# Optimization experiments

Hardware: AMD Instinct MI355X
Metric: run time of the kernel (lower is better)

Reference implementation:

```python
import jax, jax.numpy as jnp
import numpy as np

D_MODEL = 256; D_FFN = 2048; N_LEVELS = 4; N_HEADS = 8; N_POINTS = 4
B = 4; LQ = 900
SPATIAL_SHAPES = np.array([[100, 134], [50, 67], [25, 34], [13, 17]], dtype=np.int32)
LEVEL_START = np.concatenate([[0], np.cumsum(SPATIAL_SHAPES.prod(1))[:-1]]).astype(np.int32)
LV = int(SPATIAL_SHAPES.prod(1).sum())


def layer_norm(x, g, b, eps=1e-5):
    m = x.mean(-1, keepdims=True)
    v = ((x - m) ** 2).mean(-1, keepdims=True)
    return (x - m) / jnp.sqrt(v + eps) * g + b


def mha(x, in_w, in_b, out_w, out_b):
    # x: [L, B, C]  (seq-first, like nn.MultiheadAttention)
    L, Bm, C = x.shape
    dh = C // N_HEADS
    qkv = x @ in_w.T + in_b
    q, k, v = jnp.split(qkv, 3, axis=-1)
    q = q.reshape(L, Bm, N_HEADS, dh) / jnp.sqrt(jnp.asarray(dh, x.dtype))
    k = k.reshape(L, Bm, N_HEADS, dh)
    v = v.reshape(L, Bm, N_HEADS, dh)
    attn = jax.nn.softmax(jnp.einsum('lbhd,mbhd->bhlm', q, k), axis=-1)
    o = jnp.einsum('bhlm,mbhd->lbhd', attn, v).reshape(L, Bm, C)
    return o @ out_w.T + out_b


def bilinear_sample(value_l, x, y, Hl, Wl):
    # value_l: [BH, Hl*Wl, Dh]; x, y: [BH, S] in pixel coords (align_corners=False, zero pad)
    x0 = jnp.floor(x)
    y0 = jnp.floor(y)
    out = 0.0
    for dx, dy in ((0, 0), (1, 0), (0, 1), (1, 1)):
        xi = x0 + dx
        yi = y0 + dy
        wgt = (1.0 - jnp.abs(x - xi)) * (1.0 - jnp.abs(y - yi))
        valid = (xi >= 0) & (xi < Wl) & (yi >= 0) & (yi < Hl)
        xi_c = jnp.clip(xi, 0, Wl - 1).astype(jnp.int32)
        yi_c = jnp.clip(yi, 0, Hl - 1).astype(jnp.int32)
        idx = yi_c * Wl + xi_c  # [BH, S]
        v = jnp.take_along_axis(value_l, idx[..., None], axis=1)  # [BH, S, Dh]
        out = out + jnp.where(valid, wgt, 0.0)[..., None] * v
    return out


def msdeform(query, ref, mem, spatial_shapes, vproj_w, vproj_b, off_w, off_b, aw_w, aw_b, oproj_w, oproj_b):
    # query: [B, Lq, C]; ref: [B, Lq, L, 2] in [0,1]; mem: [B, Lv, C]
    Bm, Lq, C = query.shape
    Dh = C // N_HEADS
    value = (mem @ vproj_w.T + vproj_b).reshape(Bm, -1, N_HEADS, Dh)
    off = (query @ off_w.T + off_b).reshape(Bm, Lq, N_HEADS, N_LEVELS, N_POINTS, 2)
    aw = jax.nn.softmax((query @ aw_w.T + aw_b).reshape(Bm, Lq, N_HEADS, N_LEVELS * N_POINTS), axis=-1)
    aw = aw.reshape(Bm, Lq, N_HEADS, N_LEVELS, N_POINTS)
    norm = jnp.stack([spatial_shapes[:, 1], spatial_shapes[:, 0]], -1).astype(query.dtype)  # [L,2]=(W,H)
    loc = ref[:, :, None, :, None, :] + off / norm[None, None, None, :, None, :]  # [B,Lq,H,L,P,2]
    acc = jnp.zeros((Bm, Lq, N_HEADS, Dh), query.dtype)
    for l in range(N_LEVELS):
        Hl = int(SPATIAL_SHAPES[l, 0]); Wl = int(SPATIAL_SHAPES[l, 1]); s = int(LEVEL_START[l])
        v_l = value[:, s:s + Hl * Wl].transpose(0, 2, 1, 3).reshape(Bm * N_HEADS, Hl * Wl, Dh)
        x = (loc[:, :, :, l, :, 0] * Wl - 0.5).transpose(0, 2, 1, 3).reshape(Bm * N_HEADS, Lq * N_POINTS)
        y = (loc[:, :, :, l, :, 1] * Hl - 0.5).transpose(0, 2, 1, 3).reshape(Bm * N_HEADS, Lq * N_POINTS)
        sampled = bilinear_sample(v_l, x, y, Hl, Wl).reshape(Bm, N_HEADS, Lq, N_POINTS, Dh)
        acc = acc + jnp.einsum('bqhp,bhqpd->bqhd', aw[:, :, :, l], sampled)
    return acc.reshape(Bm, Lq, C) @ oproj_w.T + oproj_b


def forward_layer(tgt, tgt_reference_points, memory, memory_spatial_shapes,
                  vproj_w, vproj_b, off_w, off_b, aw_w, aw_b, oproj_w, oproj_b, ln1_g, ln1_b,
                  sa_in_w, sa_in_b, sa_out_w, sa_out_b, ln2_g, ln2_b,
                  l1_w, l1_b, l2_w, l2_b, ln3_g, ln3_b,
                  sa3_in_w, sa3_in_b, sa3_out_w, sa3_out_b, ln5_g, ln5_b,
                  l31_w, l31_b, l32_w, l32_b, ln33_g, ln33_b):
    # module_seq hardcoded in __init__: ['ca', 'sa', 'ffn', 'sa3', 'ffn3']; dropout = eval-mode identity
    # ---- ca (MSDeformAttn cross-attention) ----
    q = tgt.transpose(1, 0, 2)                                   # [B,LQ,C]
    ref = tgt_reference_points.transpose(1, 0, 2, 3)             # [B,LQ,L,2]
    mem = memory.transpose(1, 0, 2)                              # [B,LV,C]
    tgt2 = msdeform(q, ref, mem, memory_spatial_shapes, vproj_w, vproj_b, off_w, off_b,
                    aw_w, aw_b, oproj_w, oproj_b).transpose(1, 0, 2)
    tgt = layer_norm(tgt + tgt2, ln1_g, ln1_b)
    # ---- sa ----
    tgt = layer_norm(tgt + mha(tgt, sa_in_w, sa_in_b, sa_out_w, sa_out_b), ln2_g, ln2_b)
    # ---- ffn ----
    tgt = layer_norm(tgt + (jax.nn.relu(tgt @ l1_w.T + l1_b) @ l2_w.T + l2_b), ln3_g, ln3_b)
    # ---- sa3 ----
    tgt = layer_norm(tgt + mha(tgt, sa3_in_w, sa3_in_b, sa3_out_w, sa3_out_b), ln5_g, ln5_b)
    # ---- ffn3 ----
    tgt = layer_norm(tgt + (jax.nn.relu(tgt @ l31_w.T + l31_b) @ l32_w.T + l32_b), ln33_g, ln33_b)
    return tgt


def setup_inputs() -> dict:
    key = jax.random.key(0)
    ks = iter(jax.random.split(key, 48))
    def w(shape, s=0.02):
        return jax.random.normal(next(ks), shape, jnp.float32) * s
    C = D_MODEL; HLP = N_HEADS * N_LEVELS * N_POINTS
    z = lambda n: jnp.zeros((n,), jnp.float32)
    o = lambda n: jnp.ones((n,), jnp.float32)
    return {
        'tgt': w((LQ, B, C), 1.0),
        'tgt_reference_points': jax.random.uniform(next(ks), (LQ, B, N_LEVELS, 2), jnp.float32),
        'memory': w((LV, B, C), 1.0),
        'memory_spatial_shapes': jnp.asarray(SPATIAL_SHAPES),
        'memory_level_start_index': jnp.asarray(LEVEL_START),
        'vproj_w': w((C, C)), 'vproj_b': z(C),
        'off_w': w((HLP * 2, C)), 'off_b': w((HLP * 2,), 0.5),
        'aw_w': w((HLP, C)), 'aw_b': z(HLP),
        'oproj_w': w((C, C)), 'oproj_b': z(C),
        'ln1_g': o(C), 'ln1_b': z(C),
        'sa_in_w': w((3 * C, C)), 'sa_in_b': z(3 * C),
        'sa_out_w': w((C, C)), 'sa_out_b': z(C),
        'ln2_g': o(C), 'ln2_b': z(C),
        'l1_w': w((D_FFN, C)), 'l1_b': z(D_FFN),
        'l2_w': w((C, D_FFN)), 'l2_b': z(C),
        'ln3_g': o(C), 'ln3_b': z(C),
        'sa3_in_w': w((3 * C, C)), 'sa3_in_b': z(3 * C),
        'sa3_out_w': w((C, C)), 'sa3_out_b': z(C),
        'ln5_g': o(C), 'ln5_b': z(C),
        'l31_w': w((D_FFN, C)), 'l31_b': z(D_FFN),
        'l32_w': w((C, D_FFN)), 'l32_b': z(C),
        'ln33_g': o(C), 'ln33_b': z(C),
    }


def reference(tgt, tgt_reference_points, memory, memory_spatial_shapes, memory_level_start_index,
              vproj_w, vproj_b, off_w, off_b, aw_w, aw_b, oproj_w, oproj_b, ln1_g, ln1_b,
              sa_in_w, sa_in_b, sa_out_w, sa_out_b, ln2_g, ln2_b,
              l1_w, l1_b, l2_w, l2_b, ln3_g, ln3_b,
              sa3_in_w, sa3_in_b, sa3_out_w, sa3_out_b, ln5_g, ln5_b,
              l31_w, l31_b, l32_w, l32_b, ln33_g, ln33_b):
    return forward_layer(tgt, tgt_reference_points, memory, memory_spatial_shapes,
                         vproj_w, vproj_b, off_w, off_b, aw_w, aw_b, oproj_w, oproj_b, ln1_g, ln1_b,
                         sa_in_w, sa_in_b, sa_out_w, sa_out_b, ln2_g, ln2_b,
                         l1_w, l1_b, l2_w, l2_b, ln3_g, ln3_b,
                         sa3_in_w, sa3_in_b, sa3_out_w, sa3_out_b, ln5_g, ln5_b,
                         l31_w, l31_b, l32_w, l32_b, ln33_g, ln33_b)
```

## Files before the change

kernel.cpp:

```cpp
#include <hip/hip_runtime.h>
#include <math.h>

#define C 256
#define DH 32
#define NH 8
#define NL 4
#define NP 4
#define BQ 4
#define LQ 900
#define LVTOT 17821
#define DFFN 2048
#define NTOK (BQ*LQ)

typedef __attribute__((ext_vector_type(8))) short bf8_t;
typedef __attribute__((ext_vector_type(4))) float f4_t;
typedef __attribute__((ext_vector_type(8))) unsigned short us8_t;
typedef __attribute__((ext_vector_type(4))) unsigned short us4_t;

union U8 { us8_t v; unsigned int u[4]; };
union U4 { us4_t v; unsigned int u[2]; };

__device__ __forceinline__ unsigned short f2bf(float f) {
    unsigned int u = __float_as_uint(f);
    u += 0x7fffu + ((u >> 16) & 1u);
    return (unsigned short)(u >> 16);
}
__device__ __forceinline__ float b2f(unsigned short u) {
    return __uint_as_float(((unsigned int)u) << 16);
}
__device__ __forceinline__ unsigned int cvtpk(float lo, float hi) {
    unsigned int r;
    asm("v_cvt_pk_bf16_f32 %0, %1, %2" : "=v"(r) : "v"(lo), "v"(hi));
    return r;
}

#define WOFF_OFFAW   0
#define WOFF_VPROJ   98304
#define WOFF_OPROJ   163840
#define WOFF_SAIN    229376
#define WOFF_SAOUT   425984
#define WOFF_L1      491520
#define WOFF_L2      1015808
#define WOFF_SA3IN   1540096
#define WOFF_SA3OUT  1736704
#define WOFF_L31     1802240
#define WOFF_L32     2326528
#define WTOT         2850816
#define PTOT         (WTOT + 921600)

__global__ void k_prep(const float* __restrict__ off_w, const float* __restrict__ aw_w,
                       const float* __restrict__ vproj_w, const float* __restrict__ oproj_w,
                       const float* __restrict__ sa_in_w, const float* __restrict__ sa_out_w,
                       const float* __restrict__ l1_w, const float* __restrict__ l2_w,
                       const float* __restrict__ sa3_in_w, const float* __restrict__ sa3_out_w,
                       const float* __restrict__ l31_w, const float* __restrict__ l32_w,
                       const float* __restrict__ off_b, const float* __restrict__ aw_b,
                       const float* __restrict__ tgt,
                       unsigned short* __restrict__ Wbf, float* __restrict__ bias384,
                       unsigned short* __restrict__ tgtU) {
    int i = blockIdx.x * 256 + threadIdx.x;
    if (i < 384) bias384[i] = (i < 256) ? off_b[i] : aw_b[i - 256];
    if (i >= PTOT) return;
    if (i >= WTOT) { int j = i - WTOT; tgtU[j] = f2bf(tgt[j]); return; }
    const float* src; int rel;
    if      (i < WOFF_VPROJ)  { if (i < 65536) { src = off_w; rel = i; } else { src = aw_w; rel = i - 65536; } }
    else if (i < WOFF_OPROJ)  { src = vproj_w;  rel = i - WOFF_VPROJ; }
    else if (i < WOFF_SAIN)   { src = oproj_w;  rel = i - WOFF_OPROJ; }
    else if (i < WOFF_SAOUT)  { src = sa_in_w;  rel = i - WOFF_SAIN; }
    else if (i < WOFF_L1)     { src = sa_out_w; rel = i - WOFF_SAOUT; }
    else if (i < WOFF_L2)     { src = l1_w;     rel = i - WOFF_L1; }
    else if (i < WOFF_SA3IN)  { src = l2_w;     rel = i - WOFF_L2; }
    else if (i < WOFF_SA3OUT) { src = sa3_in_w; rel = i - WOFF_SA3IN; }
    else if (i < WOFF_L31)    { src = sa3_out_w; rel = i - WOFF_SA3OUT; }
    else if (i < WOFF_L32)    { src = l31_w;    rel = i - WOFF_L31; }
    else                      { src = l32_w;    rel = i - WOFF_L32; }
    Wbf[i] = f2bf(src[rel]);
}

enum { MODE_NORMAL = 0, MODE_RELU = 1, MODE_VALUE = 2, MODE_QKV = 3 };

#define LDP 40

template<int K, int KS, int NTOT, int MODE, int AB, int OB, int XCDG, int SPLITK>
__global__ void k_mgemm(const void* __restrict__ A_, const unsigned short* __restrict__ Wbf,
                        const float* __restrict__ bias, void* __restrict__ Y_,
                        void* __restrict__ Y2_, int nrows) {
    __shared__ unsigned short Ash[2][128 * LDP];
    __shared__ unsigned short Bsh[2][64 * LDP];
    int t = threadIdx.x;
    int lane = t & 63, w = t >> 6;
    int wm = w & 1, wn = w >> 1;
    int rbx, cbx, khoff = 0;
    if (SPLITK) {
        int blk = blockIdx.x;
        rbx = (blk >> 6) * 8 + (blk & 7);
        cbx = (blk >> 3) & 3;
        int half = (blk >> 5) & 1;
        khoff = half * K;
        if (half) { Y_ = Y2_; bias = nullptr; }
        if (rbx * 128 >= nrows) return;
    } else if (XCDG) {
        int blk = blockIdx.x;
        rbx = (blk >> 5) * 8 + (blk & 7);
        cbx = (blk >> 3) & 3;
        if (rbx * 128 >= nrows) return;
    } else {
        rbx = blockIdx.x;
        cbx = blockIdx.y;
    }
    int r0 = rbx * 128;
    int c0 = cbx * 64;

    f4_t acc[4][2];
#pragma unroll
    for (int mt = 0; mt < 4; ++mt)
#pragma unroll
        for (int nt = 0; nt < 2; ++nt) acc[mt][nt] = (f4_t)0.f;

    int arow = t >> 1;
    int akoff = (t & 1) * 16;
    int asrc = min(r0 + arow, nrows - 1);
    const float* aptrf = (const float*)A_ + (size_t)asrc * KS + akoff + khoff;
    const unsigned short* aptrh = (const unsigned short*)A_ + (size_t)asrc * KS + akoff + khoff;
    unsigned short* adst0 = &Ash[0][arow * LDP + akoff];
    unsigned short* adst1 = &Ash[1][arow * LDP + akoff];

    int brow = t >> 2;
    int bkoff = (t & 3) * 8;
    const unsigned short* bptr = Wbf + (size_t)(c0 + brow) * KS + bkoff + khoff;
    unsigned short* bdst0 = &Bsh[0][brow * LDP + bkoff];
    unsigned short* bdst1 = &Bsh[1][brow * LDP + bkoff];

    int lr = lane & 15, kg = lane >> 4;

    float4 fA0, fA1, fA2, fA3, gA0, gA1, gA2, gA3;
    us8_t hA0, hA1, hB0, hB1;
    us8_t wA, wB;

#define ISSUE_A(k0) do { \
        if (AB) { hA0 = *(const us8_t*)(aptrh + (k0)); hA1 = *(const us8_t*)(aptrh + (k0) + 8); } \
        else { fA0 = *(const float4*)(aptrf + (k0)); fA1 = *(const float4*)(aptrf + (k0) + 4); \
               fA2 = *(const float4*)(aptrf + (k0) + 8); fA3 = *(const float4*)(aptrf + (k0) + 12); } \
        wA = *(const us8_t*)(bptr + (k0)); } while (0)
#define ISSUE_B(k0) do { \
        if (AB) { hB0 = *(const us8_t*)(aptrh + (k0)); hB1 = *(const us8_t*)(aptrh + (k0) + 8); } \
        else { gA0 = *(const float4*)(aptrf + (k0)); gA1 = *(const float4*)(aptrf + (k0) + 4); \
               gA2 = *(const float4*)(aptrf + (k0) + 8); gA3 = *(const float4*)(aptrf + (k0) + 12); } \
        wB = *(const us8_t*)(bptr + (k0)); } while (0)
#define STORE_A(buf) do { \
        if (AB) { *(us8_t*)(adst##buf) = hA0; *(us8_t*)(adst##buf + 8) = hA1; } \
        else { U8 x, y; \
               x.u[0] = cvtpk(fA0.x, fA0.y); x.u[1] = cvtpk(fA0.z, fA0.w); \
               x.u[2] = cvtpk(fA1.x, fA1.y); x.u[3] = cvtpk(fA1.z, fA1.w); \
               y.u[0] = cvtpk(fA2.x, fA2.y); y.u[1] = cvtpk(fA2.z, fA2.w); \
               y.u[2] = cvtpk(fA3.x, fA3.y); y.u[3] = cvtpk(fA3.z, fA3.w); \
               *(us8_t*)(adst##buf) = x.v; *(us8_t*)(adst##buf + 8) = y.v; } \
        *(us8_t*)(bdst##buf) = wA; } while (0)
#define STORE_B(buf) do { \
        if (AB) { *(us8_t*)(adst##buf) = hB0; *(us8_t*)(adst##buf + 8) = hB1; } \
        else { U8 x, y; \
               x.u[0] = cvtpk(gA0.x, gA0.y); x.u[1] = cvtpk(gA0.z, gA0.w); \
               x.u[2] = cvtpk(gA1.x, gA1.y); x.u[3] = cvtpk(gA1.z, gA1.w); \
               y.u[0] = cvtpk(gA2.x, gA2.y); y.u[1] = cvtpk(gA2.z, gA2.w); \
               y.u[2] = cvtpk(gA3.x, gA3.y); y.u[3] = cvtpk(gA3.z, gA3.w); \
               *(us8_t*)(adst##buf) = x.v; *(us8_t*)(adst##buf + 8) = y.v; } \
        *(us8_t*)(bdst##buf) = wB; } while (0)
#define COMPUTE(buf) do { \
        bf8_t afr[4], bfr[2]; \
        _Pragma("unroll") \
        for (int mt = 0; mt < 4; ++mt) \
            afr[mt] = *(const bf8_t*)&Ash[buf][(wm * 64 + mt * 16 + lr) * LDP + kg * 8]; \
        _Pragma("unroll") \
        for (int nt = 0; nt < 2; ++nt) \
            bfr[nt] = *(const bf8_t*)&Bsh[buf][(wn * 32 + nt * 16 + lr) * LDP + kg * 8]; \
        _Pragma("unroll") \
        for (int mt = 0; mt < 4; ++mt) \
            _Pragma("unroll") \
            for (int nt = 0; nt < 2; ++nt) \
                acc[mt][nt] = __builtin_amdgcn_mfma_f32_16x16x32_bf16(afr[mt], bfr[nt], acc[mt][nt], 0, 0, 0); \
    } while (0)

    ISSUE_A(0);
#pragma unroll 1
    for (int k0 = 0; k0 < K; k0 += 64) {
        STORE_A(0);
        ISSUE_B(k0 + 32);
        __syncthreads();
        COMPUTE(0);
        STORE_B(1);
        if (k0 + 64 < K) ISSUE_A(k0 + 64);
        __syncthreads();
        COMPUTE(1);
    }
#undef ISSUE_A
#undef ISSUE_B
#undef STORE_A
#undef STORE_B
#undef COMPUTE

#pragma unroll
    for (int mt = 0; mt < 4; ++mt) {
#pragma unroll
        for (int nt = 0; nt < 2; ++nt) {
            int col = c0 + wn * 32 + nt * 16 + lr;
            float b0s = bias ? bias[col] : 0.f;
#pragma unroll
            for (int rr = 0; rr < 4; ++rr) {
                int row = r0 + wm * 64 + mt * 16 + kg * 4 + rr;
                if (row >= nrows) continue;
                float v = acc[mt][nt][rr] + b0s;
                size_t idx;
                if (MODE == MODE_NORMAL) {
                    idx = (size_t)row * NTOT + col;
                } else if (MODE == MODE_RELU) {
                    v = fmaxf(v, 0.f);
                    idx = (size_t)row * NTOT + col;
                } else if (MODE == MODE_VALUE) {
                    int lv = row >> 2, b = row & 3;
                    int h = col >> 5, d = col & 31;
                    idx = (((size_t)b * NH + h) * LVTOT + lv) * DH + d;
                } else {
                    int lq = row >> 2, b = row & 3;
                    int part = col >> 8, cc = col & 255;
                    int h = cc >> 5, d = cc & 31;
                    if (part == 0) v *= 0.17677669529663687f;
                    idx = (size_t)part * (BQ * NH * LQ * DH) + (((size_t)b * NH + h) * LQ + lq) * DH + d;
                }
                if (OB) ((unsigned short*)Y_)[idx] = f2bf(v);
                else    ((float*)Y_)[idx] = v;
            }
        }
    }
}

__global__ void k_sample(const float* __restrict__ trp, const float* __restrict__ offaw,
                         const unsigned short* __restrict__ value,
                         unsigned short* __restrict__ accU) {
    int r = blockIdx.x;
    int b = r & 3;
    int t = threadIdx.x;
    int h = t >> 5;
    int lane32 = t & 31;
    int l = lane32 >> 3;
    int dl = lane32 & 7;
    int d0 = dl * 4;
    const unsigned short* vb = value + ((size_t)b * NH + h) * (size_t)LVTOT * DH;

    const float* lg = offaw + (size_t)r * 384 + 256 + h * 16;
    float e0,e1,e2,e3,e4,e5,e6,e7,e8,e9,e10,e11,e12,e13,e14,e15;
    {
        float4 q0 = *(const float4*)(lg);
        float4 q1 = *(const float4*)(lg + 4);
        float4 q2 = *(const float4*)(lg + 8);
        float4 q3 = *(const float4*)(lg + 12);
        float mx = fmaxf(fmaxf(fmaxf(q0.x,q0.y),fmaxf(q0.z,q0.w)),
                   fmaxf(fmaxf(fmaxf(q1.x,q1.y),fmaxf(q1.z,q1.w)),
                   fmaxf(fmaxf(fmaxf(q2.x,q2.y),fmaxf(q2.z,q2.w)),
                         fmaxf(fmaxf(q3.x,q3.y),fmaxf(q3.z,q3.w)))));
        e0=__expf(q0.x-mx); e1=__expf(q0.y-mx); e2=__expf(q0.z-mx); e3=__expf(q0.w-mx);
        e4=__expf(q1.x-mx); e5=__expf(q1.y-mx); e6=__expf(q1.z-mx); e7=__expf(q1.w-mx);
        e8=__expf(q2.x-mx); e9=__expf(q2.y-mx); e10=__expf(q2.z-mx); e11=__expf(q2.w-mx);
        e12=__expf(q3.x-mx); e13=__expf(q3.y-mx); e14=__expf(q3.z-mx); e15=__expf(q3.w-mx);
    }
    float ssum = ((e0+e1)+(e2+e3)) + ((e4+e5)+(e6+e7)) + ((e8+e9)+(e10+e11)) + ((e12+e13)+(e14+e15));
    float sinv = 1.0f / ssum;
    float w0 = (l==0) ? e0 : (l==1) ? e4 : (l==2) ? e8  : e12;
    float w1 = (l==0) ? e1 : (l==1) ? e5 : (l==2) ? e9  : e13;
    float w2 = (l==0) ? e2 : (l==1) ? e6 : (l==2) ? e10 : e14;
    float w3 = (l==0) ? e3 : (l==1) ? e7 : (l==2) ? e11 : e15;
    w0 *= sinv; w1 *= sinv; w2 *= sinv; w3 *= sinv;

    int Hl = (l==0) ? 100 : (l==1) ? 50 : (l==2) ? 25 : 13;
    int Wl = (l==0) ? 134 : (l==1) ? 67 : (l==2) ? 34 : 17;
    int s  = (l==0) ? 0 : (l==1) ? 13400 : (l==2) ? 16750 : 17600;
    float fW = (float)Wl, fH = (float)Hl;

    float rx = trp[((size_t)r * NL + l) * 2 + 0];
    float ry = trp[((size_t)r * NL + l) * 2 + 1];
    const float* offr = offaw + (size_t)r * 384 + h * 32 + l * 8;

    float o0 = 0.f, o1 = 0.f, o2 = 0.f, o3 = 0.f;
#pragma unroll
    for (int p = 0; p < 4; ++p) {
        float ox = offr[p * 2 + 0];
        float oy = offr[p * 2 + 1];
        float wq = (p==0) ? w0 : (p==1) ? w1 : (p==2) ? w2 : w3;
        float x = (rx + ox / fW) * fW - 0.5f;
        float y = (ry + oy / fH) * fH - 0.5f;
        float x0 = floorf(x), y0 = floorf(y);
#pragma unroll
        for (int dy = 0; dy < 2; ++dy) {
#pragma unroll
            for (int dx = 0; dx < 2; ++dx) {
                float xi = x0 + dx, yi = y0 + dy;
                float wgt = (1.0f - fabsf(x - xi)) * (1.0f - fabsf(y - yi));
                bool valid = (xi >= 0.f) && (xi < fW) && (yi >= 0.f) && (yi < fH);
                int xic = min(max((int)xi, 0), Wl - 1);
                int yic = min(max((int)yi, 0), Hl - 1);
                float cw = (valid ? wgt : 0.f) * wq;
                us4_t v4 = *(const us4_t*)&vb[((size_t)(s + yic * Wl + xic)) * DH + d0];
                o0 += cw * b2f(v4[0]);
                o1 += cw * b2f(v4[1]);
                o2 += cw * b2f(v4[2]);
                o3 += cw * b2f(v4[3]);
            }
        }
    }
    o0 += __shfl_xor(o0, 8, 32); o0 += __shfl_xor(o0, 16, 32);
    o1 += __shfl_xor(o1, 8, 32); o1 += __shfl_xor(o1, 16, 32);
    o2 += __shfl_xor(o2, 8, 32); o2 += __shfl_xor(o2, 16, 32);
    o3 += __shfl_xor(o3, 8, 32); o3 += __shfl_xor(o3, 16, 32);
    if (l == 0) {
        U4 u;
        u.u[0] = cvtpk(o0, o1);
        u.u[1] = cvtpk(o2, o3);
        *(us4_t*)&accU[(size_t)r * C + h * 32 + d0] = u.v;
    }
}

__global__ void k_res_ln(const float* __restrict__ Y0, const float* __restrict__ Y1,
                         const float* __restrict__ Xres, const float* __restrict__ g,
                         const float* __restrict__ be, float* __restrict__ out,
                         unsigned short* __restrict__ outU) {
    int t = threadIdx.x, wv = t >> 6, lane = t & 63;
    int r = blockIdx.x * 4 + wv;
    float4 v = ((const float4*)(Y0 + (size_t)r * C))[lane];
    float4 x = ((const float4*)(Xres + (size_t)r * C))[lane];
    v.x += x.x; v.y += x.y; v.z += x.z; v.w += x.w;
    if (Y1) {
        float4 y1 = ((const float4*)(Y1 + (size_t)r * C))[lane];
        v.x += y1.x; v.y += y1.y; v.z += y1.z; v.w += y1.w;
    }
    float s = (v.x + v.y) + (v.z + v.w);
#pragma unroll
    for (int o = 32; o > 0; o >>= 1) s += __shfl_xor(s, o, 64);
    float mean = s * (1.0f / C);
    float4 dv = make_float4(v.x - mean, v.y - mean, v.z - mean, v.w - mean);
    float q = (dv.x * dv.x + dv.y * dv.y) + (dv.z * dv.z + dv.w * dv.w);
#pragma unroll
    for (int o = 32; o > 0; o >>= 1) q += __shfl_xor(q, o, 64);
    float rstd = rsqrtf(q * (1.0f / C) + 1e-5f);
    float4 g4 = ((const float4*)g)[lane];
    float4 b4 = ((const float4*)be)[lane];
    float4 o4 = make_float4(dv.x * rstd * g4.x + b4.x, dv.y * rstd * g4.y + b4.y,
                            dv.z * rstd * g4.z + b4.z, dv.w * rstd * g4.w + b4.w);
    ((float4*)(out + (size_t)r * C))[lane] = o4;
    if (outU) {
        U4 u;
        u.u[0] = cvtpk(o4.x, o4.y);
        u.u[1] = cvtpk(o4.z, o4.w);
        *(us4_t*)(outU + (size_t)r * C + lane * 4) = u.v;
    }
}

#define NQC3 15

__global__ __launch_bounds__(256, 1)
void k_attn3(const unsigned short* __restrict__ Q, const unsigned short* __restrict__ K,
             const unsigned short* __restrict__ V, unsigned short* __restrict__ O) {
    __shared__ unsigned short sK[4][64 * 72];
    __shared__ unsigned short sV[4][32 * 72];
    __shared__ float sPO[4][64 * 36];
    __shared__ float sWm[4][64], sWl[4][64];

    int blk = blockIdx.x;
    int bh = blk & 31;
    int qc = blk >> 5;
    int b = bh >> 3, h = bh & 7;
    int t = threadIdx.x;
    int w = t >> 6, lane = t & 63;
    int lr = lane & 15, g = lane >> 4;

    const unsigned short* Qb = Q + (size_t)bh * LQ * DH;
    const unsigned short* Kb = K + (size_t)bh * LQ * DH;
    const unsigned short* Vb = V + (size_t)bh * LQ * DH;

    unsigned short* Ks = sK[w];
    unsigned short* Vt = sV[w];
    unsigned short* Ps = (unsigned short*)sPO[w];

    bf8_t qf[4];
#pragma unroll
    for (int nt = 0; nt < 4; ++nt) {
        int qg = min(qc * 64 + nt * 16 + lr, LQ - 1);
        qf[nt] = *(const bf8_t*)(Qb + (size_t)qg * DH + g * 8);
    }

    float m[4], l[4];
    f4_t acc[2][4];
#pragma unroll
    for (int nt = 0; nt < 4; ++nt) {
        m[nt] = -3e38f; l[nt] = 0.f;
        acc[0][nt] = (f4_t)0.f; acc[1][nt] = (f4_t)0.f;
    }

    for (int ci = 0; ci < 4; ++ci) {
        int k0 = ci * 256 + w * 64;
        if (k0 >= LQ) break;
        int kgl = min(k0 + lane, LQ - 1);
        const unsigned short* kr = Kb + (size_t)kgl * DH;
        const unsigned short* vr = Vb + (size_t)kgl * DH;
#pragma unroll
        for (int i = 0; i < 4; ++i)
            *(us8_t*)&Ks[lane * 72 + i * 8] = *(const us8_t*)(kr + i * 8);
#pragma unroll
        for (int i = 0; i < 4; ++i) {
            us8_t v8 = *(const us8_t*)(vr + i * 8);
#pragma unroll
            for (int j = 0; j < 8; ++j)
                Vt[(i * 8 + j) * 72 + lane] = v8[j];
        }
        bf8_t ka[4];
#pragma unroll
        for (int mt = 0; mt < 4; ++mt)
            ka[mt] = *(const bf8_t*)&Ks[(mt * 16 + lr) * 72 + g * 8];
        f4_t st[4][4];
#pragma unroll
        for (int mt = 0; mt < 4; ++mt)
#pragma unroll
            for (int nt = 0; nt < 4; ++nt)
                st[mt][nt] = __builtin_amdgcn_mfma_f32_16x16x32_bf16(ka[mt], qf[nt], (f4_t)0.f, 0, 0, 0);
#pragma unroll
        for (int nt = 0; nt < 4; ++nt) {
            float sv[4][4];
            float cm = -3e38f;
#pragma unroll
            for (int mt = 0; mt < 4; ++mt)
#pragma unroll
                for (int rr = 0; rr < 4; ++rr) {
                    bool valid = (k0 + mt * 16 + g * 4 + rr) < LQ;
                    float s = valid ? st[mt][nt][rr] : -3e38f;
                    sv[mt][rr] = s;
                    cm = fmaxf(cm, s);
                }
            cm = fmaxf(cm, __shfl_xor(cm, 16, 64));
            cm = fmaxf(cm, __shfl_xor(cm, 32, 64));
            float mn = fmaxf(m[nt], cm);
            float sc = __expf(m[nt] - mn);
            float cs = 0.f;
#pragma unroll
            for (int mt = 0; mt < 4; ++mt) {
                float pv0 = (sv[mt][0] > -1e37f) ? __expf(sv[mt][0] - mn) : 0.f;
                float pv1 = (sv[mt][1] > -1e37f) ? __expf(sv[mt][1] - mn) : 0.f;
                float pv2 = (sv[mt][2] > -1e37f) ? __expf(sv[mt][2] - mn) : 0.f;
                float pv3 = (sv[mt][3] > -1e37f) ? __expf(sv[mt][3] - mn) : 0.f;
                cs += (pv0 + pv1) + (pv2 + pv3);
                U4 pk;
                pk.u[0] = cvtpk(pv0, pv1);
                pk.u[1] = cvtpk(pv2, pv3);
                *(us4_t*)&Ps[(nt * 16 + lr) * 72 + mt * 16 + g * 4] = pk.v;
            }
            cs += __shfl_xor(cs, 16, 64);
            cs += __shfl_xor(cs, 32, 64);
            l[nt] = l[nt] * sc + cs;
            m[nt] = mn;
            acc[0][nt] *= sc;
            acc[1][nt] *= sc;
        }
        bf8_t va[2][2];
#pragma unroll
        for (int md = 0; md < 2; ++md)
#pragma unroll
            for (int kt = 0; kt < 2; ++kt)
                va[md][kt] = *(const bf8_t*)&Vt[(md * 16 + lr) * 72 + kt * 32 + g * 8];
#pragma unroll
        for (int nt = 0; nt < 4; ++nt)
#pragma unroll
            for (int kt = 0; kt < 2; ++kt) {
                bf8_t pb = *(const bf8_t*)&Ps[(nt * 16 + lr) * 72 + kt * 32 + g * 8];
                acc[0][nt] = __builtin_amdgcn_mfma_f32_16x16x32_bf16(va[0][kt], pb, acc[0][nt], 0, 0, 0);
                acc[1][nt] = __builtin_amdgcn_mfma_f32_16x16x32_bf16(va[1][kt], pb, acc[1][nt], 0, 0, 0);
            }
    }

    if (g == 0) {
#pragma unroll
        for (int nt = 0; nt < 4; ++nt) {
            sWm[w][nt * 16 + lr] = m[nt];
            sWl[w][nt * 16 + lr] = l[nt];
        }
    }
    __syncthreads();
    float* ob = sPO[w];
#pragma unroll
    for (int nt = 0; nt < 4; ++nt) {
        int q = nt * 16 + lr;
        float M = fmaxf(fmaxf(sWm[0][q], sWm[1][q]), fmaxf(sWm[2][q], sWm[3][q]));
        float fac = __expf(m[nt] - M);
        f4_t v0 = acc[0][nt] * fac;
        f4_t v1 = acc[1][nt] * fac;
        *(f4_t*)&ob[q * 36 + g * 4] = v0;
        *(f4_t*)&ob[q * 36 + 16 + g * 4] = v1;
    }
    __syncthreads();
    {
        int q = t >> 2, d0 = (t & 3) * 8;
        int qglob = qc * 64 + q;
        if (qglob < LQ) {
            float M = fmaxf(fmaxf(sWm[0][q], sWm[1][q]), fmaxf(sWm[2][q], sWm[3][q]));
            float L = 0.f;
#pragma unroll
            for (int w2 = 0; w2 < 4; ++w2) L += sWl[w2][q] * __expf(sWm[w2][q] - M);
            float inv = 1.0f / L;
            f4_t r0 = (f4_t)0.f, r1 = (f4_t)0.f;
#pragma unroll
            for (int w2 = 0; w2 < 4; ++w2) {
                r0 += *(f4_t*)&sPO[w2][q * 36 + d0];
                r1 += *(f4_t*)&sPO[w2][q * 36 + d0 + 4];
            }
            r0 *= inv; r1 *= inv;
            U8 u;
            u.u[0] = cvtpk(r0[0], r0[1]);
            u.u[1] = cvtpk(r0[2], r0[3]);
            u.u[2] = cvtpk(r1[0], r1[1]);
            u.u[3] = cvtpk(r1[2], r1[3]);
            *(us8_t*)(O + ((size_t)(qglob * BQ + b)) * C + h * 32 + d0) = u.v;
        }
    }
}

extern "C" void kernel_launch(void* const* d_in, const int* in_sizes, int n_in,
                              void* d_out, int out_size, void* d_ws, size_t ws_size,
                              hipStream_t stream) {
    const float* tgt      = (const float*)d_in[0];
    const float* trp      = (const float*)d_in[1];
    const float* memory   = (const float*)d_in[2];
    const float* vproj_w  = (const float*)d_in[5];  const float* vproj_b  = (const float*)d_in[6];
    const float* off_w    = (const float*)d_in[7];  const float* off_b    = (const float*)d_in[8];
    const float* aw_w     = (const float*)d_in[9];  const float* aw_b     = (const float*)d_in[10];
    const float* oproj_w  = (const float*)d_in[11]; const float* oproj_b  = (const float*)d_in[12];
    const float* ln1_g    = (const float*)d_in[13]; const float* ln1_b    = (const float*)d_in[14];
    const float* sa_in_w  = (const float*)d_in[15]; const float* sa_in_b  = (const float*)d_in[16];
    const float* sa_out_w = (const float*)d_in[17]; const float* sa_out_b = (const float*)d_in[18];
    const float* ln2_g    = (const float*)d_in[19]; const float* ln2_b    = (const float*)d_in[20];
    const float* l1_w     = (const float*)d_in[21]; const float* l1_b     = (const float*)d_in[22];
    const float* l2_w     = (const float*)d_in[23]; const float* l2_b     = (const float*)d_in[24];
    const float* ln3_g    = (const float*)d_in[25]; const float* ln3_b    = (const float*)d_in[26];
    const float* sa3_in_w = (const float*)d_in[27]; const float* sa3_in_b = (const float*)d_in[28];
    const float* sa3_out_w= (const float*)d_in[29]; const float* sa3_out_b= (const float*)d_in[30];
    const float* ln5_g    = (const float*)d_in[31]; const float* ln5_b    = (const float*)d_in[32];
    const float* l31_w    = (const float*)d_in[33]; const float* l31_b    = (const float*)d_in[34];
    const float* l32_w    = (const float*)d_in[35]; const float* l32_b    = (const float*)d_in[36];
    const float* ln33_g   = (const float*)d_in[37]; const float* ln33_b   = (const float*)d_in[38];

    float* ws = (float*)d_ws;
    float* X              = ws;
    unsigned short* valueU= (unsigned short*)(ws + 921600);
    float* offaw          = ws + 10045952;
    unsigned short* accU  = (unsigned short*)(ws + 11428352);
    unsigned short* QKVu  = (unsigned short*)(ws + 12349952);
    unsigned short* Ou    = (unsigned short*)(ws + 13732352);
    unsigned short* H1u   = (unsigned short*)(ws + 14193152);
    float* Y              = ws + 17879552;
    float* Y2             = ws + 18801152;
    float* T1             = ws + 19722752;
    unsigned short* Wbf   = (unsigned short*)(ws + 20644352);
    float* bias384        = ws + 22069760;
    unsigned short* XU    = (unsigned short*)(ws + 22070144);
    unsigned short* tgtU  = (unsigned short*)(ws + 22530944);

    const int NVROWS = BQ * LVTOT;
    dim3 blk(256);
    dim3 gTok(29, 4);
    void* nullv = nullptr;

    k_prep<<<(PTOT + 255) / 256, blk, 0, stream>>>(off_w, aw_w, vproj_w, oproj_w, sa_in_w, sa_out_w,
                                                   l1_w, l2_w, sa3_in_w, sa3_out_w, l31_w, l32_w,
                                                   off_b, aw_b, tgt, Wbf, bias384, tgtU);

    k_mgemm<256, 256, 256, MODE_VALUE, 0, 1, 4, 0><<<70 * 32, blk, 0, stream>>>(memory, Wbf + WOFF_VPROJ, vproj_b, valueU, nullv, NVROWS);
    k_mgemm<256, 256, 384, MODE_NORMAL, 1, 0, 0, 0><<<dim3(29, 6), blk, 0, stream>>>(tgtU, Wbf + WOFF_OFFAW, bias384, offaw, nullv, NTOK);
    k_sample<<<NTOK, blk, 0, stream>>>(trp, offaw, valueU, accU);
    k_mgemm<256, 256, 256, MODE_NORMAL, 1, 0, 0, 0><<<gTok, blk, 0, stream>>>(accU, Wbf + WOFF_OPROJ, oproj_b, T1, nullv, NTOK);
    k_res_ln<<<NTOK / 4, blk, 0, stream>>>(T1, nullptr, tgt, ln1_g, ln1_b, X, XU);

    k_mgemm<256, 256, 768, MODE_QKV, 1, 1, 0, 0><<<dim3(29, 12), blk, 0, stream>>>(XU, Wbf + WOFF_SAIN, sa_in_b, QKVu, nullv, NTOK);
    k_attn3<<<32 * NQC3, blk, 0, stream>>>(QKVu, QKVu + 921600, QKVu + 1843200, Ou);
    k_mgemm<256, 256, 256, MODE_NORMAL, 1, 0, 0, 0><<<gTok, blk, 0, stream>>>(Ou, Wbf + WOFF_SAOUT, sa_out_b, T1, nullv, NTOK);
    k_res_ln<<<NTOK / 4, blk, 0, stream>>>(T1, nullptr, X, ln2_g, ln2_b, X, XU);

    k_mgemm<256, 256, 2048, MODE_RELU, 1, 1, 0, 0><<<dim3(29, 32), blk, 0, stream>>>(XU, Wbf + WOFF_L1, l1_b, H1u, nullv, NTOK);
    k_mgemm<1024, 2048, 256, MODE_NORMAL, 1, 0, 0, 1><<<4 * 64, blk, 0, stream>>>(H1u, Wbf + WOFF_L2, l2_b, Y, Y2, NTOK);
    k_res_ln<<<NTOK / 4, blk, 0, stream>>>(Y, Y2, X, ln3_g, ln3_b, X, XU);

    k_mgemm<256, 256, 768, MODE_QKV, 1, 1, 0, 0><<<dim3(29, 12), blk, 0, stream>>>(XU, Wbf + WOFF_SA3IN, sa3_in_b, QKVu, nullv, NTOK);
    k_attn3<<<32 * NQC3, blk, 0, stream>>>(QKVu, QKVu + 921600, QKVu + 1843200, Ou);
    k_mgemm<256, 256, 256, MODE_NORMAL, 1, 0, 0, 0><<<gTok, blk, 0, stream>>>(Ou, Wbf + WOFF_SA3OUT, sa3_out_b, T1, nullv, NTOK);
    k_res_ln<<<NTOK / 4, blk, 0, stream>>>(T1, nullptr, X, ln5_g, ln5_b, X, XU);

    k_mgemm<256, 256, 2048, MODE_RELU, 1, 1, 0, 0><<<dim3(29, 32), blk, 0, stream>>>(XU, Wbf + WOFF_L31, l31_b, H1u, nullv, NTOK);
    k_mgemm<1024, 2048, 256, MODE_NORMAL, 1, 0, 0, 1><<<4 * 64, blk, 0, stream>>>(H1u, Wbf + WOFF_L32, l32_b, Y, Y2, NTOK);
    k_res_ln<<<NTOK / 4, blk, 0, stream>>>(Y, Y2, X, ln33_g, ln33_b, (float*)d_out, nullptr);
}
```

Measured before the change: 264.8 us.

## Deepen GEMM global-load prefetch to four register stages

Restructures the GEMM main loop from a 2-stage register prefetch into a 4-stage one. Global loads for the next four K-slices are in flight while the current slice is computed from double-buffered LDS. The loop now steps K by 128 and needs K to be a multiple of 128. This hides more global memory latency at the cost of many more live registers, which could lower occupancy.

```diff
diff --git a/kernel.cpp b/kernel.cpp
--- a/kernel.cpp
+++ b/kernel.cpp
@@ -133,38 +133,25 @@
 
     int lr = lane & 15, kg = lane >> 4;
 
-    float4 fA0, fA1, fA2, fA3, gA0, gA1, gA2, gA3;
-    us8_t hA0, hA1, hB0, hB1;
-    us8_t wA, wB;
-
-#define ISSUE_A(k0) do { \
-        if (AB) { hA0 = *(const us8_t*)(aptrh + (k0)); hA1 = *(const us8_t*)(aptrh + (k0) + 8); } \
-        else { fA0 = *(const float4*)(aptrf + (k0)); fA1 = *(const float4*)(aptrf + (k0) + 4); \
-               fA2 = *(const float4*)(aptrf + (k0) + 8); fA3 = *(const float4*)(aptrf + (k0) + 12); } \
-        wA = *(const us8_t*)(bptr + (k0)); } while (0)
-#define ISSUE_B(k0) do { \
-        if (AB) { hB0 = *(const us8_t*)(aptrh + (k0)); hB1 = *(const us8_t*)(aptrh + (k0) + 8); } \
-        else { gA0 = *(const float4*)(aptrf + (k0)); gA1 = *(const float4*)(aptrf + (k0) + 4); \
-               gA2 = *(const float4*)(aptrf + (k0) + 8); gA3 = *(const float4*)(aptrf + (k0) + 12); } \
-        wB = *(const us8_t*)(bptr + (k0)); } while (0)
-#define STORE_A(buf) do { \
-        if (AB) { *(us8_t*)(adst##buf) = hA0; *(us8_t*)(adst##buf + 8) = hA1; } \
+    float4 fA_0, fA_1, fA_2, fA_3, fB_0, fB_1, fB_2, fB_3;
+    float4 fC_0, fC_1, fC_2, fC_3, fD_0, fD_1, fD_2, fD_3;
+    us8_t hA_0, hA_1, hB_0, hB_1, hC_0, hC_1, hD_0, hD_1;
+    us8_t wA, wB, wC, wD;
+
+#define ISSUE(S, k0) do { \
+        if (AB) { h##S##_0 = *(const us8_t*)(aptrh + (k0)); h##S##_1 = *(const us8_t*)(aptrh + (k0) + 8); } \
+        else { f##S##_0 = *(const float4*)(aptrf + (k0)); f##S##_1 = *(const float4*)(aptrf + (k0) + 4); \
+               f##S##_2 = *(const float4*)(aptrf + (k0) + 8); f##S##_3 = *(const float4*)(aptrf + (k0) + 12); } \
+        w##S = *(const us8_t*)(bptr + (k0)); } while (0)
+#define STORE(S, buf) do { \
+        if (AB) { *(us8_t*)(adst##buf) = h##S##_0; *(us8_t*)(adst##buf + 8) = h##S##_1; } \
         else { U8 x, y; \
-               x.u[0] = cvtpk(fA0.x, fA0.y); x.u[1] = cvtpk(fA0.z, fA0.w); \
-               x.u[2] = cvtpk(fA1.x, fA1.y); x.u[3] = cvtpk(fA1.z, fA1.w); \
-               y.u[0] = cvtpk(fA2.x, fA2.y); y.u[1] = cvtpk(fA2.z, fA2.w); \
-               y.u[2] = cvtpk(fA3.x, fA3.y); y.u[3] = cvtpk(fA3.z, fA3.w); \
+               x.u[0] = cvtpk(f##S##_0.x, f##S##_0.y); x.u[1] = cvtpk(f##S##_0.z, f##S##_0.w); \
+               x.u[2] = cvtpk(f##S##_1.x, f##S##_1.y); x.u[3] = cvtpk(f##S##_1.z, f##S##_1.w); \
+               y.u[0] = cvtpk(f##S##_2.x, f##S##_2.y); y.u[1] = cvtpk(f##S##_2.z, f##S##_2.w); \
+               y.u[2] = cvtpk(f##S##_3.x, f##S##_3.y); y.u[3] = cvtpk(f##S##_3.z, f##S##_3.w); \
                *(us8_t*)(adst##buf) = x.v; *(us8_t*)(adst##buf + 8) = y.v; } \
-        *(us8_t*)(bdst##buf) = wA; } while (0)
-#define STORE_B(buf) do { \
-        if (AB) { *(us8_t*)(adst##buf) = hB0; *(us8_t*)(adst##buf + 8) = hB1; } \
-        else { U8 x, y; \
-               x.u[0] = cvtpk(gA0.x, gA0.y); x.u[1] = cvtpk(gA0.z, gA0.w); \
-               x.u[2] = cvtpk(gA1.x, gA1.y); x.u[3] = cvtpk(gA1.z, gA1.w); \
-               y.u[0] = cvtpk(gA2.x, gA2.y); y.u[1] = cvtpk(gA2.z, gA2.w); \
-               y.u[2] = cvtpk(gA3.x, gA3.y); y.u[3] = cvtpk(gA3.z, gA3.w); \
-               *(us8_t*)(adst##buf) = x.v; *(us8_t*)(adst##buf + 8) = y.v; } \
-        *(us8_t*)(bdst##buf) = wB; } while (0)
+        *(us8_t*)(bdst##buf) = w##S; } while (0)
 #define COMPUTE(buf) do { \
         bf8_t afr[4], bfr[2]; \
         _Pragma("unroll") \
@@ -180,22 +167,28 @@
                 acc[mt][nt] = __builtin_amdgcn_mfma_f32_16x16x32_bf16(afr[mt], bfr[nt], acc[mt][nt], 0, 0, 0); \
     } while (0)
 
-    ISSUE_A(0);
+    ISSUE(A, 0); ISSUE(B, 32); ISSUE(C, 64); ISSUE(D, 96);
 #pragma unroll 1
-    for (int k0 = 0; k0 < K; k0 += 64) {
-        STORE_A(0);
-        ISSUE_B(k0 + 32);
+    for (int k0 = 0; k0 < K; k0 += 128) {
+        STORE(A, 0);
         __syncthreads();
         COMPUTE(0);
-        STORE_B(1);
-        if (k0 + 64 < K) ISSUE_A(k0 + 64);
+        if (k0 + 128 < K) ISSUE(A, k0 + 128);
+        STORE(B, 1);
         __syncthreads();
         COMPUTE(1);
-    }
-#undef ISSUE_A
-#undef ISSUE_B
-#undef STORE_A
-#undef STORE_B
+        if (k0 + 160 < K) ISSUE(B, k0 + 160);
+        STORE(C, 0);
+        __syncthreads();
+        COMPUTE(0);
+        if (k0 + 192 < K) ISSUE(C, k0 + 192);
+        STORE(D, 1);
+        __syncthreads();
+        COMPUTE(1);
+        if (k0 + 224 < K) ISSUE(D, k0 + 224);
+    }
+#undef ISSUE
+#undef STORE
 #undef COMPUTE
 
 #pragma unroll
```

New measurement: 338.6 us. 1.28x slower.
